# Kernel tuning notes

Hardware: AMD Instinct MI355X
Metric: run time of the kernel (lower is better)

The kernel has to match this reference:

```python
import jax, jax.numpy as jnp
import numpy as np

NUM_EMBEDDINGS = 1024
EMBEDDING_DIM = 256


def setup_inputs() -> dict:
    key = jax.random.key(0)
    kx, kc = jax.random.split(key)
    x = jax.random.normal(kx, (32, 256, 64, 64), dtype=jnp.float32)
    # codebook initialized uniform(-1/K, 1/K) as in the torch module
    codebook = jax.random.uniform(
        kc, (NUM_EMBEDDINGS, EMBEDDING_DIM), dtype=jnp.float32,
        minval=-1.0 / NUM_EMBEDDINGS, maxval=1.0 / NUM_EMBEDDINGS)
    return {"x": x, "codebook": codebook}


def reference(x, codebook):
    # x: (B, C, H, W) -> (B, H, W, C) -> (N, C)
    B, C, H, W = x.shape
    xf = jnp.transpose(x, (0, 2, 3, 1)).reshape(-1, C)  # (N, C)
    dist = (jnp.sum(xf * xf, axis=1, keepdims=True)
            + jnp.sum(codebook * codebook, axis=1)
            - 2.0 * jnp.matmul(xf, codebook.T))
    indices = jnp.argmin(dist, axis=1)[:, None]  # (N, 1), matches torch unsqueeze(1)
    quantized = codebook[indices[:, 0]].reshape(B, H, W, C)  # gather
    quantized = jnp.transpose(quantized, (0, 3, 1, 2))  # (B, C, H, W)
    return indices, quantized
```

## Files before the change

### kernel.cpp

```cpp
#include <hip/hip_runtime.h>
#include <stdint.h>

#define CDIM   256
#define KCODES 1024
#define HWSZ   4096
#define NROWS  131072
#define DELTA_P 4.7e-4f

#define WS_BQ    0
#define WS_IDX   4096
#define WS_CBBF  528384
#define WS_CNT   1052672
#define WS_LIST  1052800

typedef __attribute__((ext_vector_type(8))) short short8;
typedef __attribute__((ext_vector_type(4))) float f32x4;

__device__ inline unsigned short bf16rne(float f) {
    uint32_t u = __float_as_uint(f);
    u += 0x7FFF + ((u >> 16) & 1);
    return (unsigned short)(u >> 16);
}

__device__ __forceinline__ unsigned umin32(unsigned a, unsigned b) { return a < b ? a : b; }
__device__ __forceinline__ unsigned umax32(unsigned a, unsigned b) { return a > b ? a : b; }

__global__ void codesq_kernel(const float* __restrict__ cb, float* __restrict__ Bq) {
#pragma clang fp contract(off)
    int k = blockIdx.x * 256 + threadIdx.x;
    if (k >= KCODES) return;
    const float* er = cb + (size_t)k * CDIM;
    float half_s[2];
    for (int h = 0; h < 2; ++h) {
        float r[8];
        #pragma unroll
        for (int j = 0; j < 8; ++j) { float v = er[h*128 + j]; r[j] = v * v; }
        for (int i = 8; i < 128; i += 8) {
            #pragma unroll
            for (int j = 0; j < 8; ++j) { float v = er[h*128 + i + j]; float sq = v*v; r[j] = r[j] + sq; }
        }
        half_s[h] = ((r[0]+r[1]) + (r[2]+r[3])) + ((r[4]+r[5]) + (r[6]+r[7]));
    }
    Bq[k] = half_s[0] + half_s[1];
}

__global__ void cbcvt_kernel(const float* __restrict__ cb, unsigned short* __restrict__ cbbf,
                             int* __restrict__ counter) {
    int i = blockIdx.x * 256 + threadIdx.x;
    float4 v = ((const float4*)cb)[i];
    ushort4 o;
    o.x = bf16rne(v.x); o.y = bf16rne(v.y); o.z = bf16rne(v.z); o.w = bf16rne(v.w);
    ((ushort4*)cbbf)[i] = o;
    if (i == 0) *counter = 0;
}

__global__ __launch_bounds__(256, 2)
void screen_kernel(const float* __restrict__ x, const unsigned short* __restrict__ cbbf,
                   const float* __restrict__ Bq,
                   int* __restrict__ idx_out, float* __restrict__ outF,
                   int* __restrict__ flag_list, int* __restrict__ counter) {
    __shared__ unsigned short xs[64 * 264];
    __shared__ unsigned int sRed[4][64][2];

    const int t = threadIdx.x;
    const int w = t >> 6, l = t & 63;
    const int l15 = l & 15, quad = l >> 4;
    const int r0 = blockIdx.x * 64;
    const float* xbase = x + (size_t)(r0 >> 12) * (CDIM * HWSZ) + (r0 & 4095);

    {
        int cbase = (t >> 4) * 2;
        int row4  = (t & 15) * 4;
        for (int it = 0; it < 8; ++it) {
            int c = cbase + it * 32;
            float4 fa = *(const float4*)(xbase + (size_t)c * HWSZ + row4);
            float4 fb = *(const float4*)(xbase + (size_t)(c + 1) * HWSZ + row4);
            *(uint32_t*)&xs[(row4+0)*264 + c] = (uint32_t)bf16rne(fa.x) | ((uint32_t)bf16rne(fb.x) << 16);
            *(uint32_t*)&xs[(row4+1)*264 + c] = (uint32_t)bf16rne(fa.y) | ((uint32_t)bf16rne(fb.y) << 16);
            *(uint32_t*)&xs[(row4+2)*264 + c] = (uint32_t)bf16rne(fa.z) | ((uint32_t)bf16rne(fb.z) << 16);
            *(uint32_t*)&xs[(row4+3)*264 + c] = (uint32_t)bf16rne(fa.w) | ((uint32_t)bf16rne(fb.w) << 16);
        }
    }

    __syncthreads();

    short8 af[8][4];
    #pragma unroll
    for (int step = 0; step < 8; ++step)
        #pragma unroll
        for (int rf = 0; rf < 4; ++rf)
            af[step][rf] = *(const short8*)&xs[(rf*16 + l15)*264 + step*32 + quad*8];

    const unsigned short* bbase = cbbf + (size_t)(w*32 + l15) * CDIM + quad * 8;
    const int kbase = w*32 + l15;

    unsigned int K1[16], K2[16];
    #pragma unroll
    for (int i = 0; i < 16; ++i) { K1[i] = 0xFFFFFFFFu; K2[i] = 0xFFFFFFFFu; }

    for (int kt = 0; kt < 8; ++kt) {
        float bqp0 = Bq[kt*128 + kbase]      + 0.75f;
        float bqp1 = Bq[kt*128 + kbase + 16] + 0.75f;

        f32x4 acc[4][2];
        #pragma unroll
        for (int rf = 0; rf < 4; ++rf)
            #pragma unroll
            for (int cf = 0; cf < 2; ++cf) acc[rf][cf] = (f32x4){0.f, 0.f, 0.f, 0.f};

        #pragma unroll
        for (int step = 0; step < 8; ++step) {
            int koff = step * 32;
            short8 bfr0 = *(const short8*)(bbase + (size_t)(kt*128)      * CDIM + koff);
            short8 bfr1 = *(const short8*)(bbase + (size_t)(kt*128 + 16) * CDIM + koff);
            #pragma unroll
            for (int rf = 0; rf < 4; ++rf) {
                acc[rf][0] = __builtin_amdgcn_mfma_f32_16x16x32_bf16(af[step][rf], bfr0, acc[rf][0], 0, 0, 0);
                acc[rf][1] = __builtin_amdgcn_mfma_f32_16x16x32_bf16(af[step][rf], bfr1, acc[rf][1], 0, 0, 0);
            }
        }

        unsigned int kk0 = (unsigned)(kt*128 + kbase);
        unsigned int kk1 = kk0 + 16u;
        #pragma unroll
        for (int rf = 0; rf < 4; ++rf)
            #pragma unroll
            for (int reg = 0; reg < 4; ++reg) {
                int st = rf*4 + reg;
                {
                    float s = fmaf(-2.f, acc[rf][0][reg], bqp0);
                    unsigned int key = (__float_as_uint(s) & 0xFFFFFC00u) | kk0;
                    unsigned int t1 = umin32(key, K1[st]);
                    unsigned int t2 = umax32(key, K1[st]);
                    K1[st] = t1;
                    K2[st] = umin32(t2, K2[st]);
                }
                {
                    float s = fmaf(-2.f, acc[rf][1][reg], bqp1);
                    unsigned int key = (__float_as_uint(s) & 0xFFFFFC00u) | kk1;
                    unsigned int t1 = umin32(key, K1[st]);
                    unsigned int t2 = umax32(key, K1[st]);
                    K1[st] = t1;
                    K2[st] = umin32(t2, K2[st]);
                }
            }
    }

    #pragma unroll
    for (int st = 0; st < 16; ++st) {
        #pragma unroll
        for (int m = 1; m < 16; m <<= 1) {
            unsigned int o1 = (unsigned int)__shfl_xor((int)K1[st], m, 64);
            unsigned int o2 = (unsigned int)__shfl_xor((int)K2[st], m, 64);
            unsigned int n2 = umin32(umax32(K1[st], o1), umin32(K2[st], o2));
            K1[st] = umin32(K1[st], o1);
            K2[st] = n2;
        }
    }
    if (l15 == 0) {
        #pragma unroll
        for (int rf = 0; rf < 4; ++rf)
            #pragma unroll
            for (int reg = 0; reg < 4; ++reg) {
                int r = rf*16 + quad*4 + reg;
                int st = rf*4 + reg;
                sRed[w][r][0] = K1[st];
                sRed[w][r][1] = K2[st];
            }
    }
    __syncthreads();
    if (t < 64) {
        unsigned int A1 = sRed[0][t][0], A2 = sRed[0][t][1];
        #pragma unroll
        for (int ww = 1; ww < 4; ++ww) {
            unsigned int B1 = sRed[ww][t][0], B2 = sRed[ww][t][1];
            unsigned int n2 = umin32(umax32(A1, B1), umin32(A2, B2));
            A1 = umin32(A1, B1);
            A2 = n2;
        }
        int row = r0 + t;
        int k1i = (int)(A1 & 1023u);
        idx_out[row] = k1i;
        outF[row] = (float)k1i;
        float v1 = __uint_as_float(A1 & 0xFFFFFC00u);
        float v2 = __uint_as_float(A2 & 0xFFFFFC00u);
        if (!(v2 - v1 > DELTA_P)) {
            int pos = atomicAdd(counter, 1);
            flag_list[pos] = row;
        }
    }
}

__global__ __launch_bounds__(256)
void rescore_kernel(const float* __restrict__ x, const float* __restrict__ cb,
                    const float* __restrict__ Bq,
                    const int* __restrict__ flag_list, const int* __restrict__ counter,
                    int* __restrict__ idx_out, float* __restrict__ outF) {
    __shared__ float xsh[64 * 256];
    __shared__ float cbs[64 * 256];
    __shared__ float sA[64];
    __shared__ int   rows_s[64];

    int cnt = *counter;
    int nbat = (cnt + 63) >> 6;
    for (int bat = blockIdx.x; bat < nbat; bat += gridDim.x) {
        __syncthreads();
        if (threadIdx.x < 64) {
            int j = bat * 64 + threadIdx.x;
            rows_s[threadIdx.x] = (j < cnt) ? flag_list[j] : -1;
        }
        __syncthreads();
        {
            int rr = threadIdx.x >> 2;
            int c0 = (threadIdx.x & 3) * 64;
            int row = rows_s[rr]; if (row < 0) row = rows_s[0];
            const float* xr = x + (size_t)(row >> 12) * (CDIM * HWSZ) + (row & 4095);
            #pragma unroll 8
            for (int j = 0; j < 64; ++j)
                xsh[rr*256 + c0 + j] = xr[(size_t)(c0 + j) * HWSZ];
        }
        __syncthreads();
        if (threadIdx.x < 64) {
#pragma clang fp contract(off)
            const float* xr = &xsh[threadIdx.x * 256];
            float hs[2];
            for (int h = 0; h < 2; ++h) {
                float rr8[8];
                #pragma unroll
                for (int j = 0; j < 8; ++j) { float v = xr[h*128 + j]; rr8[j] = v * v; }
                for (int i = 8; i < 128; i += 8) {
                    #pragma unroll
                    for (int j = 0; j < 8; ++j) { float v = xr[h*128 + i + j]; float sq = v*v; rr8[j] = rr8[j] + sq; }
                }
                hs[h] = ((rr8[0]+rr8[1]) + (rr8[2]+rr8[3])) + ((rr8[4]+rr8[5]) + (rr8[6]+rr8[7]));
            }
            sA[threadIdx.x] = hs[0] + hs[1];
        }
        __syncthreads();

        const int rq = threadIdx.x >> 4;
        const int cq = threadIdx.x & 15;
        const int sw = cq & 7;
        float Ar[4];
        #pragma unroll
        for (int i = 0; i < 4; ++i) Ar[i] = sA[rq*4 + i];

        float bv[4]; int bk[4];
        #pragma unroll
        for (int i = 0; i < 4; ++i) { bv[i] = 3.4e38f; bk[i] = 0; }

        for (int tile = 0; tile < 16; ++tile) {
            __syncthreads();
            {
                int kc = threadIdx.x >> 2, seg = threadIdx.x & 3;
                const float* crow = cb + (size_t)(tile*64 + kc) * CDIM + seg * 64;
                float* dst = &cbs[kc * 256];
                int kw = kc & 7;
                #pragma unroll
                for (int i = 0; i < 16; ++i) {
                    int lc = seg*16 + i;
                    *(float4*)&dst[(lc ^ kw) * 4] = *(const float4*)&crow[i*4];
                }
            }
            __syncthreads();
            float bq[4];
            #pragma unroll
            for (int j = 0; j < 4; ++j) bq[j] = Bq[tile*64 + cq + j*16];

            const float* eb[4];
            #pragma unroll
            for (int j = 0; j < 4; ++j) eb[j] = &cbs[(cq + j*16) * 256];
            const float* xb[4];
            #pragma unroll
            for (int i = 0; i < 4; ++i) xb[i] = &xsh[(rq*4 + i) * 256];

            float acc[4][4];
            #pragma unroll
            for (int i = 0; i < 4; ++i)
                #pragma unroll
                for (int j = 0; j < 4; ++j) acc[i][j] = 0.f;

            #pragma unroll 2
            for (int c4 = 0; c4 < 64; ++c4) {
                int so = (c4 ^ sw) * 4;
                float4 ev[4], xv[4];
                #pragma unroll
                for (int j = 0; j < 4; ++j) ev[j] = *(const float4*)&eb[j][so];
                #pragma unroll
                for (int i = 0; i < 4; ++i) xv[i] = *(const float4*)&xb[i][c4*4];
                #pragma unroll
                for (int i = 0; i < 4; ++i)
                    #pragma unroll
                    for (int j = 0; j < 4; ++j) {
                        float a = acc[i][j];
                        a = fmaf(xv[i].x, ev[j].x, a);
                        a = fmaf(xv[i].y, ev[j].y, a);
                        a = fmaf(xv[i].z, ev[j].z, a);
                        a = fmaf(xv[i].w, ev[j].w, a);
                        acc[i][j] = a;
                    }
            }
            #pragma unroll
            for (int j = 0; j < 4; ++j) {
                int k = tile*64 + cq + j*16;
                #pragma unroll
                for (int i = 0; i < 4; ++i) {
                    float T1 = Ar[i] + bq[j];
                    float s  = T1 - 2.0f * acc[i][j];
                    if (s < bv[i]) { bv[i] = s; bk[i] = k; }
                }
            }
        }
        #pragma unroll
        for (int i = 0; i < 4; ++i) {
            float b = bv[i]; int k = bk[i];
            #pragma unroll
            for (int m = 1; m < 16; m <<= 1) {
                float ov = __shfl_xor(b, m, 64);
                int   ok = __shfl_xor(k, m, 64);
                if (ov < b || (ov == b && ok < k)) { b = ov; k = ok; }
            }
            bv[i] = b; bk[i] = k;
        }
        if (cq == 0) {
            #pragma unroll
            for (int i = 0; i < 4; ++i) {
                int row = rows_s[rq*4 + i];
                if (row >= 0) { idx_out[row] = bk[i]; outF[row] = (float)bk[i]; }
            }
        }
    }
}

__global__ __launch_bounds__(256)
void gather_kernel(const float* __restrict__ cb, const int* __restrict__ idx,
                   float* __restrict__ out) {
    __shared__ int   sIdx[64];
    __shared__ float tile[64 * 129];
    const int t  = threadIdx.x;
    const int bh = blockIdx.x;
    const int b  = bh >> 6, h = bh & 63;

    if (t < 64) {
        int id = idx[bh * 64 + t];
        sIdx[t] = id;
        out[bh * 64 + t] = (float)id;
    }
    __syncthreads();

    float* qout = out + NROWS + (size_t)b * (CDIM * HWSZ) + h * 64;

    for (int c0 = 0; c0 < CDIM; c0 += 128) {
        if (c0) __syncthreads();
        {
            int ww = t >> 2, seg = t & 3;
            const float* crow = cb + (size_t)sIdx[ww] * CDIM + c0;
            #pragma unroll
            for (int jj = 0; jj < 8; ++jj) {
                int f = seg + 4 * jj;
                float4 v = *(const float4*)(crow + 4 * f);
                float* dst = &tile[ww * 129 + 4 * f];
                dst[0] = v.x; dst[1] = v.y; dst[2] = v.z; dst[3] = v.w;
            }
        }
        __syncthreads();
        {
            int g = t >> 4, w4 = (t & 15) * 4;
            #pragma unroll
            for (int it = 0; it < 8; ++it) {
                int cl = it * 16 + g;
                float4 v;
                v.x = tile[(w4 + 0) * 129 + cl];
                v.y = tile[(w4 + 1) * 129 + cl];
                v.z = tile[(w4 + 2) * 129 + cl];
                v.w = tile[(w4 + 3) * 129 + cl];
                *(float4*)(qout + (size_t)(c0 + cl) * HWSZ + w4) = v;
            }
        }
    }
}

extern "C" void kernel_launch(void* const* d_in, const int* in_sizes, int n_in,
                              void* d_out, int out_size, void* d_ws, size_t ws_size,
                              hipStream_t stream) {
    const float* x  = (const float*)d_in[0];
    const float* cb = (const float*)d_in[1];
    char* ws = (char*)d_ws;
    float*          Bq    = (float*)(ws + WS_BQ);
    int*            idxbf = (int*)(ws + WS_IDX);
    unsigned short* cbbf  = (unsigned short*)(ws + WS_CBBF);
    int*            cnt   = (int*)(ws + WS_CNT);
    int*            list  = (int*)(ws + WS_LIST);
    float*          out   = (float*)d_out;

    codesq_kernel<<<KCODES / 256, 256, 0, stream>>>(cb, Bq);
    cbcvt_kernel <<<256, 256, 0, stream>>>(cb, cbbf, cnt);
    screen_kernel<<<NROWS / 64, 256, 0, stream>>>(x, cbbf, Bq, idxbf, out, list, cnt);
    rescore_kernel<<<2048, 256, 0, stream>>>(x, cb, Bq, list, cnt, idxbf, out);
    gather_kernel<<<32 * 64, 256, 0, stream>>>(cb, idxbf, out);
}
```

Baseline: 559.2 us.

## Split rescore codebook range across four blocks and merge via 64-bit atomicMin

The rescore pass now splits each 64-row batch's 1024-code search into four quarter-codebook work items handled by separate blocks. Each block writes its local best as a packed (ordered-float, index) key with 64-bit atomicMin into a per-flagged-row slot initialised by the screen kernel. A new fixup kernel then writes the winning indices back. This raises parallelism when few rows are flagged, so the rescore tail no longer runs on a handful of blocks. The cost is reloading x for each quarter, extra atomics, and one more kernel launch.

Result: slower. 575.1 us (+2.8%).

```diff
diff --git a/kernel.cpp b/kernel.cpp
--- a/kernel.cpp
+++ b/kernel.cpp
@@ -12,6 +12,7 @@
 #define WS_CBBF  528384
 #define WS_CNT   1052672
 #define WS_LIST  1052800
+#define WS_SLOT  1577216
 
 typedef __attribute__((ext_vector_type(8))) short short8;
 typedef __attribute__((ext_vector_type(4))) float f32x4;
@@ -24,6 +25,12 @@
 
 __device__ __forceinline__ unsigned umin32(unsigned a, unsigned b) { return a < b ? a : b; }
 __device__ __forceinline__ unsigned umax32(unsigned a, unsigned b) { return a > b ? a : b; }
+
+__device__ __forceinline__ unsigned long long packkey(float s, int k) {
+    unsigned b = __float_as_uint(s);
+    unsigned m = (b & 0x80000000u) ? ~b : (b | 0x80000000u);
+    return ((unsigned long long)m << 32) | (unsigned)k;
+}
 
 __global__ void codesq_kernel(const float* __restrict__ cb, float* __restrict__ Bq) {
 #pragma clang fp contract(off)
@@ -58,7 +65,8 @@
 void screen_kernel(const float* __restrict__ x, const unsigned short* __restrict__ cbbf,
                    const float* __restrict__ Bq,
                    int* __restrict__ idx_out, float* __restrict__ outF,
-                   int* __restrict__ flag_list, int* __restrict__ counter) {
+                   int* __restrict__ flag_list, int* __restrict__ counter,
+                   unsigned long long* __restrict__ slots) {
     __shared__ unsigned short xs[64 * 264];
     __shared__ unsigned int sRed[4][64][2];
 
@@ -187,6 +195,7 @@
         if (!(v2 - v1 > DELTA_P)) {
             int pos = atomicAdd(counter, 1);
             flag_list[pos] = row;
+            slots[pos] = 0xFFFFFFFFFFFFFFFFull;
         }
     }
 }
@@ -195,7 +204,7 @@
 void rescore_kernel(const float* __restrict__ x, const float* __restrict__ cb,
                     const float* __restrict__ Bq,
                     const int* __restrict__ flag_list, const int* __restrict__ counter,
-                    int* __restrict__ idx_out, float* __restrict__ outF) {
+                    unsigned long long* __restrict__ slots) {
     __shared__ float xsh[64 * 256];
     __shared__ float cbs[64 * 256];
     __shared__ float sA[64];
@@ -203,7 +212,10 @@
 
     int cnt = *counter;
     int nbat = (cnt + 63) >> 6;
-    for (int bat = blockIdx.x; bat < nbat; bat += gridDim.x) {
+    int nwork = nbat * 4;
+    for (int wk = blockIdx.x; wk < nwork; wk += gridDim.x) {
+        int bat = wk >> 2;
+        int wq  = wk & 3;
         __syncthreads();
         if (threadIdx.x < 64) {
             int j = bat * 64 + threadIdx.x;
@@ -249,11 +261,12 @@
         #pragma unroll
         for (int i = 0; i < 4; ++i) { bv[i] = 3.4e38f; bk[i] = 0; }
 
-        for (int tile = 0; tile < 16; ++tile) {
+        for (int tile = 0; tile < 4; ++tile) {
+            int kt0 = wq * 256 + tile * 64;
             __syncthreads();
             {
                 int kc = threadIdx.x >> 2, seg = threadIdx.x & 3;
-                const float* crow = cb + (size_t)(tile*64 + kc) * CDIM + seg * 64;
+                const float* crow = cb + (size_t)(kt0 + kc) * CDIM + seg * 64;
                 float* dst = &cbs[kc * 256];
                 int kw = kc & 7;
                 #pragma unroll
@@ -265,7 +278,7 @@
             __syncthreads();
             float bq[4];
             #pragma unroll
-            for (int j = 0; j < 4; ++j) bq[j] = Bq[tile*64 + cq + j*16];
+            for (int j = 0; j < 4; ++j) bq[j] = Bq[kt0 + cq + j*16];
 
             const float* eb[4];
             #pragma unroll
@@ -302,7 +315,7 @@
             }
             #pragma unroll
             for (int j = 0; j < 4; ++j) {
-                int k = tile*64 + cq + j*16;
+                int k = kt0 + cq + j*16;
                 #pragma unroll
                 for (int i = 0; i < 4; ++i) {
                     float T1 = Ar[i] + bq[j];
@@ -325,11 +338,24 @@
         if (cq == 0) {
             #pragma unroll
             for (int i = 0; i < 4; ++i) {
-                int row = rows_s[rq*4 + i];
-                if (row >= 0) { idx_out[row] = bk[i]; outF[row] = (float)bk[i]; }
-            }
-        }
-    }
+                int j = bat * 64 + rq*4 + i;
+                if (j < cnt) atomicMin(&slots[j], packkey(bv[i], bk[i]));
+            }
+        }
+    }
+}
+
+__global__ void fixup_kernel(const unsigned long long* __restrict__ slots,
+                             const int* __restrict__ flag_list,
+                             const int* __restrict__ counter,
+                             int* __restrict__ idx_out, float* __restrict__ outF) {
+    int cnt = *counter;
+    int t = blockIdx.x * 256 + threadIdx.x;
+    if (t >= cnt) return;
+    int row = flag_list[t];
+    int k = (int)(unsigned)(slots[t] & 0xFFFFFFFFull);
+    idx_out[row] = k;
+    outF[row] = (float)k;
 }
 
 __global__ __launch_bounds__(256)
@@ -386,16 +412,18 @@
     const float* x  = (const float*)d_in[0];
     const float* cb = (const float*)d_in[1];
     char* ws = (char*)d_ws;
-    float*          Bq    = (float*)(ws + WS_BQ);
-    int*            idxbf = (int*)(ws + WS_IDX);
-    unsigned short* cbbf  = (unsigned short*)(ws + WS_CBBF);
-    int*            cnt   = (int*)(ws + WS_CNT);
-    int*            list  = (int*)(ws + WS_LIST);
-    float*          out   = (float*)d_out;
+    float*              Bq    = (float*)(ws + WS_BQ);
+    int*                idxbf = (int*)(ws + WS_IDX);
+    unsigned short*     cbbf  = (unsigned short*)(ws + WS_CBBF);
+    int*                cnt   = (int*)(ws + WS_CNT);
+    int*                list  = (int*)(ws + WS_LIST);
+    unsigned long long* slots = (unsigned long long*)(ws + WS_SLOT);
+    float*              out   = (float*)d_out;
 
     codesq_kernel<<<KCODES / 256, 256, 0, stream>>>(cb, Bq);
     cbcvt_kernel <<<256, 256, 0, stream>>>(cb, cbbf, cnt);
-    screen_kernel<<<NROWS / 64, 256, 0, stream>>>(x, cbbf, Bq, idxbf, out, list, cnt);
-    rescore_kernel<<<2048, 256, 0, stream>>>(x, cb, Bq, list, cnt, idxbf, out);
+    screen_kernel<<<NROWS / 64, 256, 0, stream>>>(x, cbbf, Bq, idxbf, out, list, cnt, slots);
+    rescore_kernel<<<2048, 256, 0, stream>>>(x, cb, Bq, list, cnt, slots);
+    fixup_kernel <<<NROWS / 256, 256, 0, stream>>>(slots, list, cnt, idxbf, out);
     gather_kernel<<<32 * 64, 256, 0, stream>>>(cb, idxbf, out);
 }
```
